# Kernel optimization log

Hardware: AMD Instinct MI355X
Metric: run time of the kernel (lower is better)

## Reference

```python
import jax, jax.numpy as jnp
import numpy as np

C_S, C_P, FEAT_DIM, NUM_BINS = 256, 128, 64, 22
TOTAL_EDGE_FEATS = FEAT_DIM * 2 + NUM_BINS * 2 + 2  # embed_diffuse_mask=True
LN_EPS = 1e-5


def calc_distogram(pos, min_bin, max_bin, num_bins):
    # pos: [B, N, 3] -> one-hot distance bins [B, N, N, num_bins]
    d = jnp.linalg.norm(pos[:, :, None, :] - pos[:, None, :, :], axis=-1)[..., None]
    lower = jnp.linspace(min_bin, max_bin, num_bins, dtype=pos.dtype)
    upper = jnp.concatenate([lower[1:], jnp.array([1e8], dtype=pos.dtype)])
    return ((d > lower) & (d < upper)).astype(pos.dtype)


def cross_concat(f):
    # f: [B, N, D] -> [B, N, N, 2D]: row-broadcast feats then col-broadcast feats
    B, N, D = f.shape
    fi = jnp.broadcast_to(f[:, :, None, :], (B, N, N, D))
    fj = jnp.broadcast_to(f[:, None, :, :], (B, N, N, D))
    return jnp.concatenate([fi, fj], axis=-1)


def setup_inputs() -> dict:
    key = jax.random.key(0)
    ks = jax.random.split(key, 12)
    B, N = 2, 512
    inp = {
        'init_node_embed': jax.random.normal(ks[0], (B, N, C_S), jnp.float32),
        'trans_t': jax.random.normal(ks[1], (B, N, 3), jnp.float32),
        'trans_sc': jax.random.normal(ks[2], (B, N, 3), jnp.float32),
        'edge_mask': jnp.ones((B, N, N), jnp.float32),
        'diffuse_mask': jnp.ones((B, N), jnp.float32),
        # params (fan-in scaled)
        'Wsp': jax.random.normal(ks[3], (C_S, FEAT_DIM), jnp.float32) / np.sqrt(C_S),
        'bsp': jnp.zeros((FEAT_DIM,), jnp.float32),
        'W1': jax.random.normal(ks[4], (TOTAL_EDGE_FEATS, C_P), jnp.float32) / np.sqrt(TOTAL_EDGE_FEATS),
        'b1': jnp.zeros((C_P,), jnp.float32),
        'W2': jax.random.normal(ks[5], (C_P, C_P), jnp.float32) / np.sqrt(C_P),
        'b2': jnp.zeros((C_P,), jnp.float32),
        'W3': jax.random.normal(ks[6], (C_P, C_P), jnp.float32) / np.sqrt(C_P),
        'b3': jnp.zeros((C_P,), jnp.float32),
        'ln_g': jnp.ones((C_P,), jnp.float32),
        'ln_b': jnp.zeros((C_P,), jnp.float32),
    }
    return inp


def reference(init_node_embed, trans_t, trans_sc, edge_mask, diffuse_mask,
              Wsp, bsp, W1, b1, W2, b2, W3, b3, ln_g, ln_b):
    p_i = init_node_embed @ Wsp + bsp                      # [B,N,feat_dim]
    cross_node = cross_concat(p_i)                          # [B,N,N,2*feat_dim]
    dist_feats = calc_distogram(trans_t, 1e-3, 20.0, NUM_BINS)
    sc_feats = calc_distogram(trans_sc, 1e-3, 20.0, NUM_BINS)
    diff_feat = cross_concat(diffuse_mask[..., None])       # [B,N,N,2]
    feats = jnp.concatenate([cross_node, dist_feats, sc_feats, diff_feat], axis=-1)
    h = jax.nn.relu(feats @ W1 + b1)
    h = jax.nn.relu(h @ W2 + b2)
    h = h @ W3 + b3
    mu = jnp.mean(h, axis=-1, keepdims=True)
    var = jnp.mean(jnp.square(h - mu), axis=-1, keepdims=True)
    h = (h - mu) * jax.lax.rsqrt(var + LN_EPS) * ln_g + ln_b
    return h * edge_mask[..., None]
```

## Files before the change

### kernel.cpp

```cpp
#include <hip/hip_runtime.h>
#include <hip/hip_bf16.h>
#include <math.h>

#define NB 2
#define NN 512
#define CS 256
#define CP 128
#define FD 64
#define NBINS 22
#define EPB 64

typedef __attribute__((ext_vector_type(8))) short bf16x8;
typedef __attribute__((ext_vector_type(4))) short bf16x4;
typedef __attribute__((ext_vector_type(4))) float f32x4;

__device__ __forceinline__ unsigned short f2bf_rne(float x) {
    unsigned int u = __float_as_uint(x);
    unsigned int r = (u + 0x7fffu + ((u >> 16) & 1u)) >> 16;
    return (unsigned short)r;
}
__device__ __forceinline__ float bf2f(unsigned short b) {
    return __uint_as_float(((unsigned int)b) << 16);
}
__device__ __forceinline__ unsigned short f2bf(float x) {
    __hip_bfloat16 h = __float2bfloat16(x);
    unsigned short u;
    __builtin_memcpy(&u, &h, 2);
    return u;
}

__device__ __forceinline__ int bin_of(float d, float step) {
    const float fk = __fdiv_rn(__fsub_rn(d, 0.001f), step);
    int k0 = (int)fk;
    k0 = k0 < 1 ? 1 : (k0 > 20 ? 20 : k0);
    int row = -1;
    #pragma unroll
    for (int dk = -1; dk <= 1; ++dk) {
        const int k = k0 + dk;
        const float lo = __fadd_rn(0.001f, __fmul_rn((float)k, step));
        const float hi = (k == NBINS - 1)
                       ? 1e8f
                       : __fadd_rn(0.001f, __fmul_rn((float)(k + 1), step));
        row = (d > lo && d < hi) ? k : row;
    }
    return row;
}

__global__ __launch_bounds__(256) void ef_prep_kernel(
    const float* __restrict__ x,
    const float* __restrict__ diffuse,
    const float* __restrict__ Wsp,
    const float* __restrict__ bsp,
    const float* __restrict__ W1,
    const float* __restrict__ b1,
    const float* __restrict__ W2,
    const float* __restrict__ W3,
    float* __restrict__ qr,
    unsigned short* __restrict__ Wp)
{
    __shared__ float xs[CS];
    __shared__ float ps[FD];
    const int t = threadIdx.x;
    if (blockIdx.x < 1024) {
        const int n = blockIdx.x;
        xs[t] = x[(size_t)n * CS + t];
        __syncthreads();
        if (t < FD) {
            float acc = bsp[t];
            #pragma unroll 8
            for (int k = 0; k < CS; ++k)
                acc = fmaf(xs[k], Wsp[k * FD + t], acc);
            ps[t] = acc;
        }
        __syncthreads();
        const float dm = diffuse[n];
        const int c = t & (CP - 1);
        if (t < CP) {
            float acc = b1[c] + dm * W1[172 * CP + c];
            #pragma unroll 8
            for (int k = 0; k < FD; ++k)
                acc = fmaf(ps[k], W1[k * CP + c], acc);
            qr[(size_t)n * CP + c] = acc;
        } else {
            float acc = dm * W1[173 * CP + c];
            #pragma unroll 8
            for (int k = 0; k < FD; ++k)
                acc = fmaf(ps[k], W1[(FD + k) * CP + c], acc);
            qr[(size_t)(1024 + n) * CP + c] = acc;
        }
    } else {
        const int s = (blockIdx.x - 1024) * 256 + t;
        const int j    = s & 7;
        const int lane = (s >> 3) & 63;
        const int mt   = (s >> 9) & 7;
        const int ki   = s >> 12;
        const int k = 32 * ki + 8 * (lane >> 4) + j;
        const int n = 16 * mt + (lane & 15);
        const float w2 = W2[k * CP + n];
        const float w3 = W3[k * CP + n];
        const unsigned short h2 = f2bf_rne(w2);
        const unsigned short l2 = f2bf_rne(w2 - bf2f(h2));
        const unsigned short h3 = f2bf_rne(w3);
        const unsigned short l3 = f2bf_rne(w3 - bf2f(h3));
        Wp[s]         = h2;
        Wp[16384 + s] = l2;
        Wp[32768 + s] = h3;
        Wp[49152 + s] = l3;
    }
}

__global__ __launch_bounds__(256, 4) void ef_edge_kernel(
    const float* __restrict__ trans_t,
    const float* __restrict__ trans_sc,
    const float* __restrict__ edge_mask,
    const float* __restrict__ W1,
    const float* __restrict__ b2,
    const float* __restrict__ b3,
    const float* __restrict__ ln_g,
    const float* __restrict__ ln_b,
    const float* __restrict__ qr,
    const unsigned short* __restrict__ Wp,
    float* __restrict__ out)
{
    __shared__ unsigned short hb[8192];
    char* hb8 = (char*)hb;
    float* psum_s  = (float*)hb8;
    float* pqsum_s = (float*)(hb8 + 4352);
    float* mus     = (float*)(hb8 + 8704);
    float* invs    = (float*)(hb8 + 8960);

    const int t   = threadIdx.x;
    const int blk = blockIdx.x;
    const int jt  = blk & 7;
    const int i   = (blk >> 3) & (NN - 1);
    const int b   = blk >> 12;
    const int j0  = jt * EPB;
    const int nodeI  = b * NN + i;
    const int nodeJ0 = b * NN + j0;

    const int w  = t >> 6;
    const int l  = t & 63;
    const int lr = l & 15;
    const int lg = l >> 4;
    const int e1 = t >> 2;
    const int c0 = (t & 3) * 32;
    const int nj = nodeJ0 + e1;

    const float step = __fdiv_rn(__fsub_rn(20.0f, 0.001f), 21.0f);
    float dx = __fsub_rn(trans_t[nodeI * 3 + 0], trans_t[nj * 3 + 0]);
    float dy = __fsub_rn(trans_t[nodeI * 3 + 1], trans_t[nj * 3 + 1]);
    float dz = __fsub_rn(trans_t[nodeI * 3 + 2], trans_t[nj * 3 + 2]);
    const float dT = sqrtf(__fadd_rn(__fadd_rn(__fmul_rn(dx, dx), __fmul_rn(dy, dy)), __fmul_rn(dz, dz)));
    dx = __fsub_rn(trans_sc[nodeI * 3 + 0], trans_sc[nj * 3 + 0]);
    dy = __fsub_rn(trans_sc[nodeI * 3 + 1], trans_sc[nj * 3 + 1]);
    dz = __fsub_rn(trans_sc[nodeI * 3 + 2], trans_sc[nj * 3 + 2]);
    const float dS = sqrtf(__fadd_rn(__fadd_rn(__fmul_rn(dx, dx), __fmul_rn(dy, dy)), __fmul_rn(dz, dz)));
    const int kT = bin_of(dT, step);
    const int kS = bin_of(dS, step);

    {
        const float fT = (kT < 0) ? 0.0f : 1.0f;
        const float fS = (kS < 0) ? 0.0f : 1.0f;
        const float* qrow = qr + (size_t)nodeI * CP + c0;
        const float* rrow = qr + (size_t)(1024 + nj) * CP + c0;
        const float* wTr  = W1 + (size_t)(kT < 0 ? 0 : 128 + kT) * CP + c0;
        const float* wSr  = W1 + (size_t)(kS < 0 ? 0 : 150 + kS) * CP + c0;
        #pragma unroll
        for (int ch = 0; ch < 4; ++ch) {
            const int cc = ch * 8;
            const float4 qa = *(const float4*)(qrow + cc);
            const float4 qb = *(const float4*)(qrow + cc + 4);
            const float4 ra = *(const float4*)(rrow + cc);
            const float4 rb = *(const float4*)(rrow + cc + 4);
            const float4 ta = *(const float4*)(wTr + cc);
            const float4 tb = *(const float4*)(wTr + cc + 4);
            const float4 sa = *(const float4*)(wSr + cc);
            const float4 sb = *(const float4*)(wSr + cc + 4);
            float h[8];
            h[0] = fmaxf(qa.x + ra.x + fT * ta.x + fS * sa.x, 0.0f);
            h[1] = fmaxf(qa.y + ra.y + fT * ta.y + fS * sa.y, 0.0f);
            h[2] = fmaxf(qa.z + ra.z + fT * ta.z + fS * sa.z, 0.0f);
            h[3] = fmaxf(qa.w + ra.w + fT * ta.w + fS * sa.w, 0.0f);
            h[4] = fmaxf(qb.x + rb.x + fT * tb.x + fS * sb.x, 0.0f);
            h[5] = fmaxf(qb.y + rb.y + fT * tb.y + fS * sb.y, 0.0f);
            h[6] = fmaxf(qb.z + rb.z + fT * tb.z + fS * sb.z, 0.0f);
            h[7] = fmaxf(qb.w + rb.w + fT * tb.w + fS * sb.w, 0.0f);
            bf16x8 H;
            #pragma unroll
            for (int u = 0; u < 8; ++u)
                H[u] = (short)f2bf(h[u]);
            const unsigned int ad = (unsigned int)e1 * 256 +
                (((unsigned int)(2 * (c0 + cc))) ^ (((unsigned int)e1 & 7) << 4));
            *(bf16x8*)(hb8 + ad) = H;
        }
    }
    __syncthreads();

    f32x4 acc[2][4];
    #pragma unroll
    for (int mt = 0; mt < 2; ++mt) {
        const float4 bv = *(const float4*)&b2[16 * (2 * w + mt) + 4 * lg];
        #pragma unroll
        for (int nt = 0; nt < 4; ++nt) {
            acc[mt][nt][0] = bv.x; acc[mt][nt][1] = bv.y;
            acc[mt][nt][2] = bv.z; acc[mt][nt][3] = bv.w;
        }
    }
    #pragma unroll
    for (int ki = 0; ki < 4; ++ki) {
        bf16x8 ah[2], al[2];
        #pragma unroll
        for (int mt = 0; mt < 2; ++mt) {
            const size_t off = (((size_t)ki * 8 + (2 * w + mt)) * 64 + l) * 8;
            ah[mt] = *(const bf16x8*)(Wp + off);
            al[mt] = *(const bf16x8*)(Wp + 16384 + off);
        }
        bf16x8 bh[4];
        #pragma unroll
        for (int nt = 0; nt < 4; ++nt) {
            const int e = 16 * nt + lr;
            const unsigned int ad = (unsigned int)e * 256 +
                (((unsigned int)(64 * ki + 16 * lg)) ^ (((unsigned int)e & 7) << 4));
            bh[nt] = *(const bf16x8*)(hb8 + ad);
        }
        __builtin_amdgcn_s_setprio(1);
        #pragma unroll
        for (int mt = 0; mt < 2; ++mt)
            #pragma unroll
            for (int nt = 0; nt < 4; ++nt) {
                acc[mt][nt] = __builtin_amdgcn_mfma_f32_16x16x32_bf16(ah[mt], bh[nt], acc[mt][nt], 0, 0, 0);
                acc[mt][nt] = __builtin_amdgcn_mfma_f32_16x16x32_bf16(al[mt], bh[nt], acc[mt][nt], 0, 0, 0);
            }
        __builtin_amdgcn_s_setprio(0);
    }
    __syncthreads();

    #pragma unroll
    for (int mt = 0; mt < 2; ++mt) {
        const int mtg = 2 * w + mt;
        #pragma unroll
        for (int nt = 0; nt < 4; ++nt) {
            const int e = 16 * nt + lr;
            bf16x4 H;
            H[0] = (short)f2bf(fmaxf(acc[mt][nt][0], 0.0f));
            H[1] = (short)f2bf(fmaxf(acc[mt][nt][1], 0.0f));
            H[2] = (short)f2bf(fmaxf(acc[mt][nt][2], 0.0f));
            H[3] = (short)f2bf(fmaxf(acc[mt][nt][3], 0.0f));
            const unsigned int ad = (unsigned int)e * 256 +
                (((unsigned int)(32 * mtg + 8 * lg)) ^ (((unsigned int)e & 7) << 4));
            *(bf16x4*)(hb8 + ad) = H;
        }
    }
    __syncthreads();

    #pragma unroll
    for (int mt = 0; mt < 2; ++mt) {
        const float4 bv = *(const float4*)&b3[16 * (2 * w + mt) + 4 * lg];
        #pragma unroll
        for (int nt = 0; nt < 4; ++nt) {
            acc[mt][nt][0] = bv.x; acc[mt][nt][1] = bv.y;
            acc[mt][nt][2] = bv.z; acc[mt][nt][3] = bv.w;
        }
    }
    #pragma unroll
    for (int ki = 0; ki < 4; ++ki) {
        bf16x8 ah[2], al[2];
        #pragma unroll
        for (int mt = 0; mt < 2; ++mt) {
            const size_t off = (((size_t)ki * 8 + (2 * w + mt)) * 64 + l) * 8;
            ah[mt] = *(const bf16x8*)(Wp + 32768 + off);
            al[mt] = *(const bf16x8*)(Wp + 49152 + off);
        }
        bf16x8 bh[4];
        #pragma unroll
        for (int nt = 0; nt < 4; ++nt) {
            const int e = 16 * nt + lr;
            const unsigned int ad = (unsigned int)e * 256 +
                (((unsigned int)(64 * ki + 16 * lg)) ^ (((unsigned int)e & 7) << 4));
            bh[nt] = *(const bf16x8*)(hb8 + ad);
        }
        __builtin_amdgcn_s_setprio(1);
        #pragma unroll
        for (int mt = 0; mt < 2; ++mt)
            #pragma unroll
            for (int nt = 0; nt < 4; ++nt) {
                acc[mt][nt] = __builtin_amdgcn_mfma_f32_16x16x32_bf16(ah[mt], bh[nt], acc[mt][nt], 0, 0, 0);
                acc[mt][nt] = __builtin_amdgcn_mfma_f32_16x16x32_bf16(al[mt], bh[nt], acc[mt][nt], 0, 0, 0);
            }
        __builtin_amdgcn_s_setprio(0);
    }
    __syncthreads();

    #pragma unroll
    for (int nt = 0; nt < 4; ++nt) {
        const int e = 16 * nt + lr;
        float s = 0.0f, s2 = 0.0f;
        #pragma unroll
        for (int mt = 0; mt < 2; ++mt)
            #pragma unroll
            for (int r = 0; r < 4; ++r) {
                const float v = acc[mt][nt][r];
                s += v;
                s2 = fmaf(v, v, s2);
            }
        psum_s[e * 17 + 4 * w + lg]  = s;
        pqsum_s[e * 17 + 4 * w + lg] = s2;
    }
    __syncthreads();

    {
        const int e = t & 63;
        float s = 0.0f, s2 = 0.0f;
        #pragma unroll
        for (int k = 0; k < 16; ++k) {
            s  += psum_s[e * 17 + k];
            s2 += pqsum_s[e * 17 + k];
        }
        const float mu  = s * (1.0f / 128.0f);
        const float var = s2 * (1.0f / 128.0f) - mu * mu;
        mus[e]  = mu;
        invs[e] = rsqrtf(var + 1e-5f);
    }
    __syncthreads();

    {
        float4 g4[2], bb4[2];
        #pragma unroll
        for (int mt = 0; mt < 2; ++mt) {
            const int n0 = 16 * (2 * w + mt) + 4 * lg;
            g4[mt]  = *(const float4*)&ln_g[n0];
            bb4[mt] = *(const float4*)&ln_b[n0];
        }
        #pragma unroll
        for (int nt = 0; nt < 4; ++nt) {
            const int e = 16 * nt + lr;
            const size_t erow = ((size_t)(b * NN + i)) * NN + (j0 + e);
            const float em  = edge_mask[erow];
            const float mu  = mus[e];
            const float inv = invs[e];
            float* op = out + erow * CP;
            #pragma unroll
            for (int mt = 0; mt < 2; ++mt) {
                const int n0 = 16 * (2 * w + mt) + 4 * lg;
                float4 o;
                o.x = ((acc[mt][nt][0] - mu) * inv * g4[mt].x + bb4[mt].x) * em;
                o.y = ((acc[mt][nt][1] - mu) * inv * g4[mt].y + bb4[mt].y) * em;
                o.z = ((acc[mt][nt][2] - mu) * inv * g4[mt].z + bb4[mt].z) * em;
                o.w = ((acc[mt][nt][3] - mu) * inv * g4[mt].w + bb4[mt].w) * em;
                *(float4*)(op + n0) = o;
            }
        }
    }
}

extern "C" void kernel_launch(void* const* d_in, const int* in_sizes, int n_in,
                              void* d_out, int out_size, void* d_ws, size_t ws_size,
                              hipStream_t stream) {
    const float* init_node = (const float*)d_in[0];
    const float* trans_t   = (const float*)d_in[1];
    const float* trans_sc  = (const float*)d_in[2];
    const float* edge_mask = (const float*)d_in[3];
    const float* diffuse   = (const float*)d_in[4];
    const float* Wsp       = (const float*)d_in[5];
    const float* bsp       = (const float*)d_in[6];
    const float* W1        = (const float*)d_in[7];
    const float* b1        = (const float*)d_in[8];
    const float* W2        = (const float*)d_in[9];
    const float* b2        = (const float*)d_in[10];
    const float* W3        = (const float*)d_in[11];
    const float* b3        = (const float*)d_in[12];
    const float* ln_g      = (const float*)d_in[13];
    const float* ln_b      = (const float*)d_in[14];
    float* out = (float*)d_out;
    float* qr  = (float*)d_ws;
    unsigned short* Wp = (unsigned short*)((char*)d_ws + (1 << 20));

    ef_prep_kernel<<<1024 + 64, 256, 0, stream>>>(
        init_node, diffuse, Wsp, bsp, W1, b1, W2, W3, qr, Wp);
    ef_edge_kernel<<<NB * NN * (NN / EPB), 256, 0, stream>>>(
        trans_t, trans_sc, edge_mask, W1, b2, b3, ln_g, ln_b, qr, Wp, out);
}
```

Measured before the change: 202.2 us.

## Process two edge tiles per block with interleaved ping-pong stages

Each block now handles two 64-edge tiles using two shared buffers and staggers their stages, so one tile's layer-1 build, GEMMs and layernorm steps are interleaved with the other tile's MFMA work between barriers. The aim is to hide global loads and LDS traffic behind matrix math and to halve the grid size. The cost is double the shared memory (32KB), two accumulator sets that raise register pressure, and possibly lower occupancy under launch_bounds(256,4).

```diff
diff --git a/kernel.cpp b/kernel.cpp
--- a/kernel.cpp
+++ b/kernel.cpp
@@ -44,6 +44,206 @@
         row = (d > lo && d < hi) ? k : row;
     }
     return row;
+}
+
+__device__ __forceinline__ void calc_bins(const float* __restrict__ tt,
+                                          const float* __restrict__ ts,
+                                          int nodeI, int nj, float step,
+                                          int& kT, int& kS) {
+    float dx = __fsub_rn(tt[nodeI * 3 + 0], tt[nj * 3 + 0]);
+    float dy = __fsub_rn(tt[nodeI * 3 + 1], tt[nj * 3 + 1]);
+    float dz = __fsub_rn(tt[nodeI * 3 + 2], tt[nj * 3 + 2]);
+    const float dT = sqrtf(__fadd_rn(__fadd_rn(__fmul_rn(dx, dx), __fmul_rn(dy, dy)), __fmul_rn(dz, dz)));
+    dx = __fsub_rn(ts[nodeI * 3 + 0], ts[nj * 3 + 0]);
+    dy = __fsub_rn(ts[nodeI * 3 + 1], ts[nj * 3 + 1]);
+    dz = __fsub_rn(ts[nodeI * 3 + 2], ts[nj * 3 + 2]);
+    const float dS = sqrtf(__fadd_rn(__fadd_rn(__fmul_rn(dx, dx), __fmul_rn(dy, dy)), __fmul_rn(dz, dz)));
+    kT = bin_of(dT, step);
+    kS = bin_of(dS, step);
+}
+
+__device__ __forceinline__ void build_h1(char* __restrict__ buf,
+                                         const float* __restrict__ qr,
+                                         const float* __restrict__ W1,
+                                         int nodeI, int nj, int kT, int kS,
+                                         int e1, int c0) {
+    const float fT = (kT < 0) ? 0.0f : 1.0f;
+    const float fS = (kS < 0) ? 0.0f : 1.0f;
+    const float* qrow = qr + (size_t)nodeI * CP + c0;
+    const float* rrow = qr + (size_t)(1024 + nj) * CP + c0;
+    const float* wTr  = W1 + (size_t)(kT < 0 ? 0 : 128 + kT) * CP + c0;
+    const float* wSr  = W1 + (size_t)(kS < 0 ? 0 : 150 + kS) * CP + c0;
+    #pragma unroll
+    for (int ch = 0; ch < 4; ++ch) {
+        const int cc = ch * 8;
+        const float4 qa = *(const float4*)(qrow + cc);
+        const float4 qb = *(const float4*)(qrow + cc + 4);
+        const float4 ra = *(const float4*)(rrow + cc);
+        const float4 rb = *(const float4*)(rrow + cc + 4);
+        const float4 ta = *(const float4*)(wTr + cc);
+        const float4 tb = *(const float4*)(wTr + cc + 4);
+        const float4 sa = *(const float4*)(wSr + cc);
+        const float4 sb = *(const float4*)(wSr + cc + 4);
+        float h[8];
+        h[0] = fmaxf(qa.x + ra.x + fT * ta.x + fS * sa.x, 0.0f);
+        h[1] = fmaxf(qa.y + ra.y + fT * ta.y + fS * sa.y, 0.0f);
+        h[2] = fmaxf(qa.z + ra.z + fT * ta.z + fS * sa.z, 0.0f);
+        h[3] = fmaxf(qa.w + ra.w + fT * ta.w + fS * sa.w, 0.0f);
+        h[4] = fmaxf(qb.x + rb.x + fT * tb.x + fS * sb.x, 0.0f);
+        h[5] = fmaxf(qb.y + rb.y + fT * tb.y + fS * sb.y, 0.0f);
+        h[6] = fmaxf(qb.z + rb.z + fT * tb.z + fS * sb.z, 0.0f);
+        h[7] = fmaxf(qb.w + rb.w + fT * tb.w + fS * sb.w, 0.0f);
+        bf16x8 H;
+        #pragma unroll
+        for (int u = 0; u < 8; ++u)
+            H[u] = (short)f2bf(h[u]);
+        const unsigned int ad = (unsigned int)e1 * 256 +
+            (((unsigned int)(2 * (c0 + cc))) ^ (((unsigned int)e1 & 7) << 4));
+        *(bf16x8*)(buf + ad) = H;
+    }
+}
+
+__device__ __forceinline__ void gemm_layer(f32x4 acc[2][4],
+                                           const char* __restrict__ buf,
+                                           const unsigned short* __restrict__ WpH,
+                                           const unsigned short* __restrict__ WpL,
+                                           const float* __restrict__ bias,
+                                           int w, int l, int lr, int lg) {
+    #pragma unroll
+    for (int mt = 0; mt < 2; ++mt) {
+        const float4 bv = *(const float4*)&bias[16 * (2 * w + mt) + 4 * lg];
+        #pragma unroll
+        for (int nt = 0; nt < 4; ++nt) {
+            acc[mt][nt][0] = bv.x; acc[mt][nt][1] = bv.y;
+            acc[mt][nt][2] = bv.z; acc[mt][nt][3] = bv.w;
+        }
+    }
+    #pragma unroll
+    for (int ki = 0; ki < 4; ++ki) {
+        bf16x8 ah[2], al[2];
+        #pragma unroll
+        for (int mt = 0; mt < 2; ++mt) {
+            const size_t off = (((size_t)ki * 8 + (2 * w + mt)) * 64 + l) * 8;
+            ah[mt] = *(const bf16x8*)(WpH + off);
+            al[mt] = *(const bf16x8*)(WpL + off);
+        }
+        bf16x8 bh[4];
+        #pragma unroll
+        for (int nt = 0; nt < 4; ++nt) {
+            const int e = 16 * nt + lr;
+            const unsigned int ad = (unsigned int)e * 256 +
+                (((unsigned int)(64 * ki + 16 * lg)) ^ (((unsigned int)e & 7) << 4));
+            bh[nt] = *(const bf16x8*)(buf + ad);
+        }
+        __builtin_amdgcn_s_setprio(1);
+        #pragma unroll
+        for (int mt = 0; mt < 2; ++mt)
+            #pragma unroll
+            for (int nt = 0; nt < 4; ++nt) {
+                acc[mt][nt] = __builtin_amdgcn_mfma_f32_16x16x32_bf16(ah[mt], bh[nt], acc[mt][nt], 0, 0, 0);
+                acc[mt][nt] = __builtin_amdgcn_mfma_f32_16x16x32_bf16(al[mt], bh[nt], acc[mt][nt], 0, 0, 0);
+            }
+        __builtin_amdgcn_s_setprio(0);
+    }
+}
+
+__device__ __forceinline__ void store_h2(char* __restrict__ buf,
+                                         const f32x4 acc[2][4],
+                                         int w, int lr, int lg) {
+    #pragma unroll
+    for (int mt = 0; mt < 2; ++mt) {
+        const int mtg = 2 * w + mt;
+        #pragma unroll
+        for (int nt = 0; nt < 4; ++nt) {
+            const int e = 16 * nt + lr;
+            bf16x4 H;
+            H[0] = (short)f2bf(fmaxf(acc[mt][nt][0], 0.0f));
+            H[1] = (short)f2bf(fmaxf(acc[mt][nt][1], 0.0f));
+            H[2] = (short)f2bf(fmaxf(acc[mt][nt][2], 0.0f));
+            H[3] = (short)f2bf(fmaxf(acc[mt][nt][3], 0.0f));
+            const unsigned int ad = (unsigned int)e * 256 +
+                (((unsigned int)(32 * mtg + 8 * lg)) ^ (((unsigned int)e & 7) << 4));
+            *(bf16x4*)(buf + ad) = H;
+        }
+    }
+}
+
+__device__ __forceinline__ void ln_part(char* __restrict__ scr,
+                                        const f32x4 acc[2][4],
+                                        int w, int lr, int lg) {
+    float* psum_s  = (float*)scr;
+    float* pqsum_s = (float*)(scr + 4352);
+    #pragma unroll
+    for (int nt = 0; nt < 4; ++nt) {
+        const int e = 16 * nt + lr;
+        float s = 0.0f, s2 = 0.0f;
+        #pragma unroll
+        for (int mt = 0; mt < 2; ++mt)
+            #pragma unroll
+            for (int r = 0; r < 4; ++r) {
+                const float v = acc[mt][nt][r];
+                s += v;
+                s2 = fmaf(v, v, s2);
+            }
+        psum_s[e * 17 + 4 * w + lg]  = s;
+        pqsum_s[e * 17 + 4 * w + lg] = s2;
+    }
+}
+
+__device__ __forceinline__ void ln_red(char* __restrict__ scr, int t) {
+    float* psum_s  = (float*)scr;
+    float* pqsum_s = (float*)(scr + 4352);
+    float* mus     = (float*)(scr + 8704);
+    float* invs    = (float*)(scr + 8960);
+    const int e = t & 63;
+    float s = 0.0f, s2 = 0.0f;
+    #pragma unroll
+    for (int k = 0; k < 16; ++k) {
+        s  += psum_s[e * 17 + k];
+        s2 += pqsum_s[e * 17 + k];
+    }
+    const float mu  = s * (1.0f / 128.0f);
+    const float var = s2 * (1.0f / 128.0f) - mu * mu;
+    mus[e]  = mu;
+    invs[e] = rsqrtf(var + 1e-5f);
+}
+
+__device__ __forceinline__ void store_out(float* __restrict__ out,
+                                          const float* __restrict__ edge_mask,
+                                          const float* __restrict__ ln_g,
+                                          const float* __restrict__ ln_b,
+                                          const f32x4 acc[2][4],
+                                          const char* __restrict__ scr,
+                                          int b, int i, int j0,
+                                          int w, int lr, int lg) {
+    const float* mus  = (const float*)(scr + 8704);
+    const float* invs = (const float*)(scr + 8960);
+    float4 g4[2], bb4[2];
+    #pragma unroll
+    for (int mt = 0; mt < 2; ++mt) {
+        const int n0 = 16 * (2 * w + mt) + 4 * lg;
+        g4[mt]  = *(const float4*)&ln_g[n0];
+        bb4[mt] = *(const float4*)&ln_b[n0];
+    }
+    #pragma unroll
+    for (int nt = 0; nt < 4; ++nt) {
+        const int e = 16 * nt + lr;
+        const size_t erow = ((size_t)(b * NN + i)) * NN + (j0 + e);
+        const float em  = edge_mask[erow];
+        const float mu  = mus[e];
+        const float inv = invs[e];
+        float* op = out + erow * CP;
+        #pragma unroll
+        for (int mt = 0; mt < 2; ++mt) {
+            const int n0 = 16 * (2 * w + mt) + 4 * lg;
+            float4 o;
+            o.x = ((acc[mt][nt][0] - mu) * inv * g4[mt].x + bb4[mt].x) * em;
+            o.y = ((acc[mt][nt][1] - mu) * inv * g4[mt].y + bb4[mt].y) * em;
+            o.z = ((acc[mt][nt][2] - mu) * inv * g4[mt].z + bb4[mt].z) * em;
+            o.w = ((acc[mt][nt][3] - mu) * inv * g4[mt].w + bb4[mt].w) * em;
+            *(float4*)(op + n0) = o;
+        }
+    }
 }
 
 __global__ __launch_bounds__(256) void ef_prep_kernel(
@@ -122,21 +322,18 @@
     const unsigned short* __restrict__ Wp,
     float* __restrict__ out)
 {
-    __shared__ unsigned short hb[8192];
-    char* hb8 = (char*)hb;
-    float* psum_s  = (float*)hb8;
-    float* pqsum_s = (float*)(hb8 + 4352);
-    float* mus     = (float*)(hb8 + 8704);
-    float* invs    = (float*)(hb8 + 8960);
+    __shared__ char hb8[32768];
+    char* bufA = hb8;
+    char* bufB = hb8 + 16384;
 
     const int t   = threadIdx.x;
     const int blk = blockIdx.x;
-    const int jt  = blk & 7;
-    const int i   = (blk >> 3) & (NN - 1);
-    const int b   = blk >> 12;
-    const int j0  = jt * EPB;
-    const int nodeI  = b * NN + i;
-    const int nodeJ0 = b * NN + j0;
+    const int jtp = blk & 3;
+    const int i   = (blk >> 2) & (NN - 1);
+    const int b   = blk >> 11;
+    const int j0A = jtp * 128;
+    const int j0B = j0A + 64;
+    const int nodeI = b * NN + i;
 
     const int w  = t >> 6;
     const int l  = t & 63;
@@ -144,213 +341,45 @@
     const int lg = l >> 4;
     const int e1 = t >> 2;
     const int c0 = (t & 3) * 32;
-    const int nj = nodeJ0 + e1;
+    const int njA = b * NN + j0A + e1;
+    const int njB = b * NN + j0B + e1;
 
     const float step = __fdiv_rn(__fsub_rn(20.0f, 0.001f), 21.0f);
-    float dx = __fsub_rn(trans_t[nodeI * 3 + 0], trans_t[nj * 3 + 0]);
-    float dy = __fsub_rn(trans_t[nodeI * 3 + 1], trans_t[nj * 3 + 1]);
-    float dz = __fsub_rn(trans_t[nodeI * 3 + 2], trans_t[nj * 3 + 2]);
-    const float dT = sqrtf(__fadd_rn(__fadd_rn(__fmul_rn(dx, dx), __fmul_rn(dy, dy)), __fmul_rn(dz, dz)));
-    dx = __fsub_rn(trans_sc[nodeI * 3 + 0], trans_sc[nj * 3 + 0]);
-    dy = __fsub_rn(trans_sc[nodeI * 3 + 1], trans_sc[nj * 3 + 1]);
-    dz = __fsub_rn(trans_sc[nodeI * 3 + 2], trans_sc[nj * 3 + 2]);
-    const float dS = sqrtf(__fadd_rn(__fadd_rn(__fmul_rn(dx, dx), __fmul_rn(dy, dy)), __fmul_rn(dz, dz)));
-    const int kT = bin_of(dT, step);
-    const int kS = bin_of(dS, step);
-
-    {
-        const float fT = (kT < 0) ? 0.0f : 1.0f;
-        const float fS = (kS < 0) ? 0.0f : 1.0f;
-        const float* qrow = qr + (size_t)nodeI * CP + c0;
-        const float* rrow = qr + (size_t)(1024 + nj) * CP + c0;
-        const float* wTr  = W1 + (size_t)(kT < 0 ? 0 : 128 + kT) * CP + c0;
-        const float* wSr  = W1 + (size_t)(kS < 0 ? 0 : 150 + kS) * CP + c0;
-        #pragma unroll
-        for (int ch = 0; ch < 4; ++ch) {
-            const int cc = ch * 8;
-            const float4 qa = *(const float4*)(qrow + cc);
-            const float4 qb = *(const float4*)(qrow + cc + 4);
-            const float4 ra = *(const float4*)(rrow + cc);
-            const float4 rb = *(const float4*)(rrow + cc + 4);
-            const float4 ta = *(const float4*)(wTr + cc);
-            const float4 tb = *(const float4*)(wTr + cc + 4);
-            const float4 sa = *(const float4*)(wSr + cc);
-            const float4 sb = *(const float4*)(wSr + cc + 4);
-            float h[8];
-            h[0] = fmaxf(qa.x + ra.x + fT * ta.x + fS * sa.x, 0.0f);
-            h[1] = fmaxf(qa.y + ra.y + fT * ta.y + fS * sa.y, 0.0f);
-            h[2] = fmaxf(qa.z + ra.z + fT * ta.z + fS * sa.z, 0.0f);
-            h[3] = fmaxf(qa.w + ra.w + fT * ta.w + fS * sa.w, 0.0f);
-            h[4] = fmaxf(qb.x + rb.x + fT * tb.x + fS * sb.x, 0.0f);
-            h[5] = fmaxf(qb.y + rb.y + fT * tb.y + fS * sb.y, 0.0f);
-            h[6] = fmaxf(qb.z + rb.z + fT * tb.z + fS * sb.z, 0.0f);
-            h[7] = fmaxf(qb.w + rb.w + fT * tb.w + fS * sb.w, 0.0f);
-            bf16x8 H;
-            #pragma unroll
-            for (int u = 0; u < 8; ++u)
-                H[u] = (short)f2bf(h[u]);
-            const unsigned int ad = (unsigned int)e1 * 256 +
-                (((unsigned int)(2 * (c0 + cc))) ^ (((unsigned int)e1 & 7) << 4));
-            *(bf16x8*)(hb8 + ad) = H;
-        }
-    }
-    __syncthreads();
-
-    f32x4 acc[2][4];
-    #pragma unroll
-    for (int mt = 0; mt < 2; ++mt) {
-        const float4 bv = *(const float4*)&b2[16 * (2 * w + mt) + 4 * lg];
-        #pragma unroll
-        for (int nt = 0; nt < 4; ++nt) {
-            acc[mt][nt][0] = bv.x; acc[mt][nt][1] = bv.y;
-            acc[mt][nt][2] = bv.z; acc[mt][nt][3] = bv.w;
-        }
-    }
-    #pragma unroll
-    for (int ki = 0; ki < 4; ++ki) {
-        bf16x8 ah[2], al[2];
-        #pragma unroll
-        for (int mt = 0; mt < 2; ++mt) {
-            const size_t off = (((size_t)ki * 8 + (2 * w + mt)) * 64 + l) * 8;
-            ah[mt] = *(const bf16x8*)(Wp + off);
-            al[mt] = *(const bf16x8*)(Wp + 16384 + off);
-        }
-        bf16x8 bh[4];
-        #pragma unroll
-        for (int nt = 0; nt < 4; ++nt) {
-            const int e = 16 * nt + lr;
-            const unsigned int ad = (unsigned int)e * 256 +
-                (((unsigned int)(64 * ki + 16 * lg)) ^ (((unsigned int)e & 7) << 4));
-            bh[nt] = *(const bf16x8*)(hb8 + ad);
-        }
-        __builtin_amdgcn_s_setprio(1);
-        #pragma unroll
-        for (int mt = 0; mt < 2; ++mt)
-            #pragma unroll
-            for (int nt = 0; nt < 4; ++nt) {
-                acc[mt][nt] = __builtin_amdgcn_mfma_f32_16x16x32_bf16(ah[mt], bh[nt], acc[mt][nt], 0, 0, 0);
-                acc[mt][nt] = __builtin_amdgcn_mfma_f32_16x16x32_bf16(al[mt], bh[nt], acc[mt][nt], 0, 0, 0);
-            }
-        __builtin_amdgcn_s_setprio(0);
-    }
-    __syncthreads();
-
-    #pragma unroll
-    for (int mt = 0; mt < 2; ++mt) {
-        const int mtg = 2 * w + mt;
-        #pragma unroll
-        for (int nt = 0; nt < 4; ++nt) {
-            const int e = 16 * nt + lr;
-            bf16x4 H;
-            H[0] = (short)f2bf(fmaxf(acc[mt][nt][0], 0.0f));
-            H[1] = (short)f2bf(fmaxf(acc[mt][nt][1], 0.0f));
-            H[2] = (short)f2bf(fmaxf(acc[mt][nt][2], 0.0f));
-            H[3] = (short)f2bf(fmaxf(acc[mt][nt][3], 0.0f));
-            const unsigned int ad = (unsigned int)e * 256 +
-                (((unsigned int)(32 * mtg + 8 * lg)) ^ (((unsigned int)e & 7) << 4));
-            *(bf16x4*)(hb8 + ad) = H;
-        }
-    }
-    __syncthreads();
-
-    #pragma unroll
-    for (int mt = 0; mt < 2; ++mt) {
-        const float4 bv = *(const float4*)&b3[16 * (2 * w + mt) + 4 * lg];
-        #pragma unroll
-        for (int nt = 0; nt < 4; ++nt) {
-            acc[mt][nt][0] = bv.x; acc[mt][nt][1] = bv.y;
-            acc[mt][nt][2] = bv.z; acc[mt][nt][3] = bv.w;
-        }
-    }
-    #pragma unroll
-    for (int ki = 0; ki < 4; ++ki) {
-        bf16x8 ah[2], al[2];
-        #pragma unroll
-        for (int mt = 0; mt < 2; ++mt) {
-            const size_t off = (((size_t)ki * 8 + (2 * w + mt)) * 64 + l) * 8;
-            ah[mt] = *(const bf16x8*)(Wp + 32768 + off);
-            al[mt] = *(const bf16x8*)(Wp + 49152 + off);
-        }
-        bf16x8 bh[4];
-        #pragma unroll
-        for (int nt = 0; nt < 4; ++nt) {
-            const int e = 16 * nt + lr;
-            const unsigned int ad = (unsigned int)e * 256 +
-                (((unsigned int)(64 * ki + 16 * lg)) ^ (((unsigned int)e & 7) << 4));
-            bh[nt] = *(const bf16x8*)(hb8 + ad);
-        }
-        __builtin_amdgcn_s_setprio(1);
-        #pragma unroll
-        for (int mt = 0; mt < 2; ++mt)
-            #pragma unroll
-            for (int nt = 0; nt < 4; ++nt) {
-                acc[mt][nt] = __builtin_amdgcn_mfma_f32_16x16x32_bf16(ah[mt], bh[nt], acc[mt][nt], 0, 0, 0);
-                acc[mt][nt] = __builtin_amdgcn_mfma_f32_16x16x32_bf16(al[mt], bh[nt], acc[mt][nt], 0, 0, 0);
-            }
-        __builtin_amdgcn_s_setprio(0);
-    }
-    __syncthreads();
-
-    #pragma unroll
-    for (int nt = 0; nt < 4; ++nt) {
-        const int e = 16 * nt + lr;
-        float s = 0.0f, s2 = 0.0f;
-        #pragma unroll
-        for (int mt = 0; mt < 2; ++mt)
-            #pragma unroll
-            for (int r = 0; r < 4; ++r) {
-                const float v = acc[mt][nt][r];
-                s += v;
-                s2 = fmaf(v, v, s2);
-            }
-        psum_s[e * 17 + 4 * w + lg]  = s;
-        pqsum_s[e * 17 + 4 * w + lg] = s2;
-    }
-    __syncthreads();
-
-    {
-        const int e = t & 63;
-        float s = 0.0f, s2 = 0.0f;
-        #pragma unroll
-        for (int k = 0; k < 16; ++k) {
-            s  += psum_s[e * 17 + k];
-            s2 += pqsum_s[e * 17 + k];
-        }
-        const float mu  = s * (1.0f / 128.0f);
-        const float var = s2 * (1.0f / 128.0f) - mu * mu;
-        mus[e]  = mu;
-        invs[e] = rsqrtf(var + 1e-5f);
-    }
-    __syncthreads();
-
-    {
-        float4 g4[2], bb4[2];
-        #pragma unroll
-        for (int mt = 0; mt < 2; ++mt) {
-            const int n0 = 16 * (2 * w + mt) + 4 * lg;
-            g4[mt]  = *(const float4*)&ln_g[n0];
-            bb4[mt] = *(const float4*)&ln_b[n0];
-        }
-        #pragma unroll
-        for (int nt = 0; nt < 4; ++nt) {
-            const int e = 16 * nt + lr;
-            const size_t erow = ((size_t)(b * NN + i)) * NN + (j0 + e);
-            const float em  = edge_mask[erow];
-            const float mu  = mus[e];
-            const float inv = invs[e];
-            float* op = out + erow * CP;
-            #pragma unroll
-            for (int mt = 0; mt < 2; ++mt) {
-                const int n0 = 16 * (2 * w + mt) + 4 * lg;
-                float4 o;
-                o.x = ((acc[mt][nt][0] - mu) * inv * g4[mt].x + bb4[mt].x) * em;
-                o.y = ((acc[mt][nt][1] - mu) * inv * g4[mt].y + bb4[mt].y) * em;
-                o.z = ((acc[mt][nt][2] - mu) * inv * g4[mt].z + bb4[mt].z) * em;
-                o.w = ((acc[mt][nt][3] - mu) * inv * g4[mt].w + bb4[mt].w) * em;
-                *(float4*)(op + n0) = o;
-            }
-        }
-    }
+
+    int kTA, kSA;
+    calc_bins(trans_t, trans_sc, nodeI, njA, step, kTA, kSA);
+    build_h1(bufA, qr, W1, nodeI, njA, kTA, kSA, e1, c0);
+    __syncthreads();
+
+    int kTB, kSB;
+    calc_bins(trans_t, trans_sc, nodeI, njB, step, kTB, kSB);
+    f32x4 accA[2][4];
+    gemm_layer(accA, bufA, Wp, Wp + 16384, b2, w, l, lr, lg);
+    build_h1(bufB, qr, W1, nodeI, njB, kTB, kSB, e1, c0);
+    __syncthreads();
+
+    store_h2(bufA, accA, w, lr, lg);
+    f32x4 accB[2][4];
+    gemm_layer(accB, bufB, Wp, Wp + 16384, b2, w, l, lr, lg);
+    __syncthreads();
+
+    store_h2(bufB, accB, w, lr, lg);
+    gemm_layer(accA, bufA, Wp + 32768, Wp + 49152, b3, w, l, lr, lg);
+    __syncthreads();
+
+    ln_part(bufA, accA, w, lr, lg);
+    gemm_layer(accB, bufB, Wp + 32768, Wp + 49152, b3, w, l, lr, lg);
+    __syncthreads();
+
+    ln_red(bufA, t);
+    ln_part(bufB, accB, w, lr, lg);
+    __syncthreads();
+
+    store_out(out, edge_mask, ln_g, ln_b, accA, bufA, b, i, j0A, w, lr, lg);
+    ln_red(bufB, t);
+    __syncthreads();
+
+    store_out(out, edge_mask, ln_g, ln_b, accB, bufB, b, i, j0B, w, lr, lg);
 }
 
 extern "C" void kernel_launch(void* const* d_in, const int* in_sizes, int n_in,
@@ -377,6 +406,6 @@
 
     ef_prep_kernel<<<1024 + 64, 256, 0, stream>>>(
         init_node, diffuse, Wsp, bsp, W1, b1, W2, W3, qr, Wp);
-    ef_edge_kernel<<<NB * NN * (NN / EPB), 256, 0, stream>>>(
+    ef_edge_kernel<<<NB * NN * (NN / EPB / 2), 256, 0, stream>>>(
         trans_t, trans_sc, edge_mask, W1, b2, b3, ln_g, ln_b, qr, Wp, out);
 }
```

Measured after the change: 288.4 us. 1.43x slower.
